# Optimization experiments

Hardware: AMD Instinct MI355X
Metric: run time of the kernel (lower is better)

The kernel has to match this reference:

```python
import jax, jax.numpy as jnp
import numpy as np
from jax import lax

EPS = 1e-4

def whatever_norm(z):
    m = jnp.mean(z, axis=-1, keepdims=True)
    v = jnp.var(z, axis=-1, keepdims=True)
    return (z - m) * lax.rsqrt(v + EPS)

def attend_layer(x_seq, speech, Ua_W, Ua_b, Wa_W, Wa_b, va_W, va_b, K, R, b):
    # x_seq: [B, T, U], speech: [B, Te, E]
    B = x_seq.shape[0]
    units = R.shape[0]
    enc = speech @ Ua_W + Ua_b  # [B, Te, U]  (Ua(speech_encode))

    def step(carry, x_t):
        h, c = carry
        s = h @ Wa_W + Wa_b                                   # Wa(states[0]) [B,U]
        logits = jnp.squeeze(jnp.tanh(s[:, None, :] + enc) @ va_W + va_b, -1)  # [B,Te]
        w = jax.nn.softmax(logits, axis=-1)
        ctx = jnp.einsum('bt,bte->be', w, speech)             # context [B,E]
        z = jnp.concatenate([x_t, ctx], axis=1) @ K + h @ R + b
        i, f, g, o = jnp.split(z, 4, axis=1)                  # keras gate order i,f,c,o
        i = jax.nn.sigmoid(i); f = jax.nn.sigmoid(f); o = jax.nn.sigmoid(o)
        c_new = f * c + i * jnp.tanh(g)
        h_new = o * jnp.tanh(c_new)
        return (h_new, c_new), h_new

    h0 = jnp.zeros((B, units), x_seq.dtype)
    _, ys = lax.scan(step, (h0, h0), jnp.swapaxes(x_seq, 0, 1))
    return jnp.swapaxes(ys, 0, 1)  # [B, T, U]


def setup_inputs() -> dict:
    key = jax.random.key(0)
    ks = iter(jax.random.split(key, 40))
    B, Td, Te, E, U, NC = 64, 512, 1024, 512, 256, 64
    g = lambda *s: (jax.random.normal(next(ks), s, dtype=jnp.float32) * (1.0 / np.sqrt(s[0])))
    inp = {
        'trans': jax.random.normal(next(ks), (B, Td, NC), dtype=jnp.float32),
        'speech': jax.random.normal(next(ks), (B, Te, E), dtype=jnp.float32),
        'emb_W': g(NC, U), 'emb_b': jnp.zeros((U,), jnp.float32),
    }
    for L in ('1', '2'):
        inp['Ua%s_W' % L] = g(E, U); inp['Ua%s_b' % L] = jnp.zeros((U,), jnp.float32)
        inp['Wa%s_W' % L] = g(U, U); inp['Wa%s_b' % L] = jnp.zeros((U,), jnp.float32)
        inp['va%s_W' % L] = g(U, 1); inp['va%s_b' % L] = jnp.zeros((1,), jnp.float32)
        inp['K%s' % L] = g(U + E, 4 * U)
        inp['R%s' % L] = g(U, 4 * U)
        # bias_initializer_two_cell: zeros for i, 2.0 for f, zeros for c and o
        inp['b%s' % L] = jnp.concatenate([
            jnp.zeros((U,)), 2.0 * jnp.ones((U,)), jnp.zeros((2 * U,))]).astype(jnp.float32)
    inp['m1_W'] = g(U, U); inp['m1_b'] = jnp.zeros((U,), jnp.float32)
    inp['m2_W'] = g(U, U); inp['m2_b'] = jnp.zeros((U,), jnp.float32)
    inp['d_W'] = g(U, NC); inp['d_b'] = jnp.zeros((NC,), jnp.float32)
    return inp


def reference(trans, speech, emb_W, emb_b,
              Ua1_W, Ua1_b, Wa1_W, Wa1_b, va1_W, va1_b, K1, R1, b1,
              Ua2_W, Ua2_b, Wa2_W, Wa2_b, va2_W, va2_b, K2, R2, b2,
              m1_W, m1_b, m2_W, m2_b, d_W, d_b):
    secrets = trans @ emb_W + emb_b
    out = attend_layer(secrets, speech, Ua1_W, Ua1_b, Wa1_W, Wa1_b, va1_W, va1_b, K1, R1, b1)
    out = whatever_norm(out)
    out = attend_layer(out, speech, Ua2_W, Ua2_b, Wa2_W, Wa2_b, va2_W, va2_b, K2, R2, b2)
    out = whatever_norm(out)
    out = whatever_norm(out @ m1_W + m1_b)
    out = whatever_norm(out @ m2_W + m2_b)
    return jax.nn.softmax(out @ d_W + d_b, axis=-1)
```

## Files before the change

kernel.cpp:

```cpp
#include <hip/hip_runtime.h>
#include <hip/hip_bf16.h>
#include <stdint.h>

#define B  64
#define TD 512
#define TE 1024
#define EE 512
#define UU 256

__device__ __forceinline__ float fexp2(float x){ return __builtin_amdgcn_exp2f(x); }
__device__ __forceinline__ float frcp_(float x){ return __builtin_amdgcn_rcpf(x); }
__device__ __forceinline__ float tanh_fast(float x){
  float e = fexp2(x * 2.885390082f);
  return 1.f - 2.f * frcp_(e + 1.f);
}
__device__ __forceinline__ float sigmoid_fast(float x){
  return frcp_(1.f + fexp2(-1.442695041f * x));
}
__device__ __forceinline__ unsigned short f2bf(float f){
  unsigned int u = __float_as_uint(f);
  u = (u + 0x7fffu + ((u >> 16) & 1u)) >> 16;
  return (unsigned short)u;
}
__device__ __forceinline__ float bflo(unsigned int w){ return __uint_as_float(w << 16); }
__device__ __forceinline__ float bfhi(unsigned int w){ return __uint_as_float(w & 0xffff0000u); }

__device__ __forceinline__ void gstore(float* p, float v){
  __hip_atomic_store(p, v, __ATOMIC_RELAXED, __HIP_MEMORY_SCOPE_SYSTEM);
}
__device__ __forceinline__ float gload(const float* p){
  return __hip_atomic_load(p, __ATOMIC_RELAXED, __HIP_MEMORY_SCOPE_SYSTEM);
}
__device__ __forceinline__ void drain_stores(){
  __atomic_signal_fence(__ATOMIC_SEQ_CST);
  __builtin_amdgcn_s_waitcnt(0);
  __atomic_signal_fence(__ATOMIC_SEQ_CST);
}

template<int NITER>
__device__ __forceinline__ void gate_accum8(const unsigned short* __restrict__ KRP,
    const float* catp, float* zb, int q8, int k0, int tid, int lane){
  const int c = tid & 15, kg = tid >> 4;
  const uint4* kp = (const uint4*)KRP + ((size_t)q8*1024 + k0 + kg*NITER)*16 + c;
  float a0=0.f,a1=0.f,a2=0.f,a3=0.f,a4=0.f,a5=0.f,a6=0.f,a7=0.f;
  #pragma unroll 4
  for (int i = 0; i < NITER; ++i){
    uint4 w = kp[(size_t)i*16];
    float ck = catp[k0 + kg*NITER + i];
    a0 += ck*bflo(w.x); a1 += ck*bfhi(w.x);
    a2 += ck*bflo(w.y); a3 += ck*bfhi(w.y);
    a4 += ck*bflo(w.z); a5 += ck*bfhi(w.z);
    a6 += ck*bflo(w.w); a7 += ck*bfhi(w.w);
  }
  a0 += __shfl_xor(a0, 16); a1 += __shfl_xor(a1, 16);
  a2 += __shfl_xor(a2, 16); a3 += __shfl_xor(a3, 16);
  a4 += __shfl_xor(a4, 16); a5 += __shfl_xor(a5, 16);
  a6 += __shfl_xor(a6, 16); a7 += __shfl_xor(a7, 16);
  a0 += __shfl_xor(a0, 32); a1 += __shfl_xor(a1, 32);
  a2 += __shfl_xor(a2, 32); a3 += __shfl_xor(a3, 32);
  a4 += __shfl_xor(a4, 32); a5 += __shfl_xor(a5, 32);
  a6 += __shfl_xor(a6, 32); a7 += __shfl_xor(a7, 32);
  if (lane < 16){
    atomicAdd(&zb[c*8+0], a0); atomicAdd(&zb[c*8+1], a1);
    atomicAdd(&zb[c*8+2], a2); atomicAdd(&zb[c*8+3], a3);
    atomicAdd(&zb[c*8+4], a4); atomicAdd(&zb[c*8+5], a5);
    atomicAdd(&zb[c*8+6], a6); atomicAdd(&zb[c*8+7], a7);
  }
}

__global__ void pack_bf16v(const float* __restrict__ in, unsigned short* __restrict__ out, int n4){
  int i = blockIdx.x * blockDim.x + threadIdx.x;
  int stride = gridDim.x * blockDim.x;
  for (; i < n4; i += stride){
    float4 v = ((const float4*)in)[i];
    ushort4 o;
    o.x = f2bf(v.x); o.y = f2bf(v.y); o.z = f2bf(v.z); o.w = f2bf(v.w);
    ((ushort4*)out)[i] = o;
  }
}

__global__ void pack_KRP(const float* __restrict__ K, const float* __restrict__ R,
                         unsigned short* __restrict__ KRP){
  int idx = blockIdx.x * 256 + threadIdx.x;
  int q8 = idx >> 17;
  int k  = (idx >> 7) & 1023;
  int jj = idx & 127;
  int J  = (jj >> 5)*256 + q8*32 + (jj & 31);
  float v = (k < 768) ? K[(size_t)k*1024 + J] : R[(size_t)(k - 768)*1024 + J];
  KRP[idx] = f2bf(v);
}

__global__ __launch_bounds__(256) void emb_gemm(const float* __restrict__ trans,
    const float* __restrict__ W, const float* __restrict__ bias, float* __restrict__ out){
  __shared__ __align__(16) float aT[64*20];
  const int row0 = blockIdx.x * 16;
  const int tid = threadIdx.x;
  {
    int r = tid >> 6, k = tid & 63;
    for (int rr = r; rr < 16; rr += 4)
      aT[k*20 + rr] = trans[(size_t)(row0 + rr)*64 + k];
  }
  __syncthreads();
  const int j = tid;
  float bj = bias[j];
  float acc[16];
  #pragma unroll
  for (int r = 0; r < 16; ++r) acc[r] = bj;
  for (int k = 0; k < 64; ++k){
    float w = W[(size_t)k*UU + j];
    const float4* a4 = (const float4*)(aT + k*20);
    float4 q0 = a4[0], q1 = a4[1], q2 = a4[2], q3 = a4[3];
    acc[0]+=q0.x*w;  acc[1]+=q0.y*w;  acc[2]+=q0.z*w;  acc[3]+=q0.w*w;
    acc[4]+=q1.x*w;  acc[5]+=q1.y*w;  acc[6]+=q1.z*w;  acc[7]+=q1.w*w;
    acc[8]+=q2.x*w;  acc[9]+=q2.y*w;  acc[10]+=q2.z*w; acc[11]+=q2.w*w;
    acc[12]+=q3.x*w; acc[13]+=q3.y*w; acc[14]+=q3.z*w; acc[15]+=q3.w*w;
  }
  #pragma unroll
  for (int r = 0; r < 16; ++r)
    out[(size_t)(row0 + r)*UU + j] = acc[r];
}

__global__ __launch_bounds__(256) void enc_gemm(const float* __restrict__ speech,
    const float* __restrict__ Ua, const float* __restrict__ Uab,
    unsigned short* __restrict__ enc){
  __shared__ __align__(16) float aT[512*20];
  const int wg = blockIdx.x;
  const int b = wg >> 6, tb = (wg & 63) * 16;
  const int tid = threadIdx.x;
  const float* sp = speech + ((size_t)b*TE + tb)*EE;
  for (int it = 0; it < 32; ++it){
    int idx = tid + 256*it;
    int te = idx >> 9, e = idx & 511;
    aT[e*20 + te] = sp[(size_t)te*EE + e];
  }
  __syncthreads();
  const int j = tid;
  float bj = Uab[j];
  float acc[16];
  #pragma unroll
  for (int r = 0; r < 16; ++r) acc[r] = bj;
  const float* up = Ua + j;
  for (int e = 0; e < 512; ++e){
    float w = up[(size_t)e*UU];
    const float4* a4 = (const float4*)(aT + e*20);
    float4 q0 = a4[0], q1 = a4[1], q2 = a4[2], q3 = a4[3];
    acc[0]+=q0.x*w;  acc[1]+=q0.y*w;  acc[2]+=q0.z*w;  acc[3]+=q0.w*w;
    acc[4]+=q1.x*w;  acc[5]+=q1.y*w;  acc[6]+=q1.z*w;  acc[7]+=q1.w*w;
    acc[8]+=q2.x*w;  acc[9]+=q2.y*w;  acc[10]+=q2.z*w; acc[11]+=q2.w*w;
    acc[12]+=q3.x*w; acc[13]+=q3.y*w; acc[14]+=q3.z*w; acc[15]+=q3.w*w;
  }
  unsigned short* op = enc + ((size_t)b*TE + tb)*UU + j;
  #pragma unroll
  for (int r = 0; r < 16; ++r) op[(size_t)r*UU] = f2bf(acc[r]);
}

__global__ __launch_bounds__(512)
__attribute__((amdgpu_waves_per_eu(4, 4)))
void scan_kernel(
    const float* __restrict__ x_seq, float* __restrict__ y_out,
    const unsigned short* __restrict__ enc, const unsigned short* __restrict__ speech,
    const unsigned short* __restrict__ KRP, const unsigned short* __restrict__ Wab,
    const float* __restrict__ Wa_b, const float* __restrict__ va,
    const float* __restrict__ gate_b,
    float* __restrict__ pctx_g, float* __restrict__ l_g, float* __restrict__ h_g,
    unsigned int* __restrict__ ctr){
  extern __shared__ __align__(16) unsigned short enc_l[];
  __shared__ float2 sva[256];
  __shared__ float cat[1024];
  __shared__ float c_lds[32];
  __shared__ float lds_logit4[512];
  __shared__ float p_lds[128];
  __shared__ float lds_pctx[512];
  __shared__ float zbuf[2][128];
  __shared__ float s_acc[256];
  __shared__ float red[16];
  __shared__ float nmi[2];

  const int tid = threadIdx.x;
  const int wg = blockIdx.x;
  const int b = wg >> 3, q8 = wg & 7;
  const int lane = tid & 63, wave = tid >> 6;
  unsigned int bar = 0;
  unsigned int* cptr = &ctr[b*16];

  {
    const uint4* ep4 = (const uint4*)(enc + ((size_t)b*TE + q8*128)*UU);
    #pragma unroll
    for (int i = 0; i < 8; ++i){
      int idx = tid + 512*i;
      int te_l = idx >> 5, ch = idx & 31;
      uint4 v = ep4[(size_t)te_l*32 + ch];
      *(uint4*)(enc_l + (size_t)te_l*264 + ch*8) = v;
    }
  }
  if (tid < 256){ sva[tid] = make_float2(Wa_b[tid], va[tid]); cat[768 + tid] = 0.f; }
  if (tid < 128){ zbuf[0][tid] = 0.f; zbuf[1][tid] = 0.f; }
  if (tid < 32) c_lds[tid] = 0.f;
  if (tid >= 256 && tid < 512)
    cat[tid - 256] = x_seq[((size_t)b*TD + 0)*UU + (tid - 256)];
  __syncthreads();
  gate_accum8<8>(KRP, cat, zbuf[0], q8, 0, tid, lane);

  for (int t = 0; t < TD; ++t){
    lds_pctx[tid] = 0.f;
    if (tid < 128) zbuf[(t+1)&1][tid] = 0.f;
    if (tid < 256) s_acc[tid] = 0.f;
    float xnext = 0.f;
    if (t < TD-1 && tid >= 256 && tid < 512)
      xnext = x_seq[((size_t)b*TD + t + 1)*UU + (tid - 256)];
    __syncthreads();

    {
      const int g = wave & 1, r = wave >> 1;
      const int te_l = g*64 + lane;
      const unsigned short* ep = enc_l + (size_t)te_l*264 + r*64;
      float acc = 0.f;
      #pragma unroll
      for (int c = 0; c < 8; ++c){
        uint4 v = *(const uint4*)(ep + c*8);
        const int ub = r*64 + c*8;
        unsigned int wv[4] = {v.x, v.y, v.z, v.w};
        #pragma unroll
        for (int i = 0; i < 4; ++i){
          float2 s0 = sva[ub + 2*i];
          float2 s1 = sva[ub + 2*i + 1];
          acc += s0.y * tanh_fast(s0.x + bflo(wv[i]));
          acc += s1.y * tanh_fast(s1.x + bfhi(wv[i]));
        }
      }
      lds_logit4[r*128 + te_l] = acc;
    }
    __syncthreads();

    if (tid < 128){
      float lg = lds_logit4[tid] + lds_logit4[128 + tid]
               + lds_logit4[256 + tid] + lds_logit4[384 + tid];
      float p = fexp2(lg * 1.442695041f);
      p_lds[tid] = p;
      float s = p;
      #pragma unroll
      for (int o = 32; o > 0; o >>= 1) s += __shfl_xor(s, o);
      if (lane == 0) red[wave] = s;
    }
    __syncthreads();

    {
      const int c = tid & 63, tg = tid >> 6;
      const uint4* sp4 = (const uint4*)speech + ((size_t)b*TE + q8*128 + tg*16)*64 + c;
      float a0=0.f,a1=0.f,a2=0.f,a3=0.f,a4=0.f,a5=0.f,a6=0.f,a7=0.f;
      #pragma unroll 4
      for (int i = 0; i < 16; ++i){
        uint4 w = sp4[(size_t)i*64];
        float p = p_lds[tg*16 + i];
        a0 += p*bflo(w.x); a1 += p*bfhi(w.x);
        a2 += p*bflo(w.y); a3 += p*bfhi(w.y);
        a4 += p*bflo(w.z); a5 += p*bfhi(w.z);
        a6 += p*bflo(w.w); a7 += p*bfhi(w.w);
      }
      atomicAdd(&lds_pctx[c*8+0], a0); atomicAdd(&lds_pctx[c*8+1], a1);
      atomicAdd(&lds_pctx[c*8+2], a2); atomicAdd(&lds_pctx[c*8+3], a3);
      atomicAdd(&lds_pctx[c*8+4], a4); atomicAdd(&lds_pctx[c*8+5], a5);
      atomicAdd(&lds_pctx[c*8+6], a6); atomicAdd(&lds_pctx[c*8+7], a7);
    }
    __syncthreads();
    gstore(&pctx_g[((size_t)(b*8 + q8))*512 + tid], lds_pctx[tid]);
    if (tid == 0)  gstore(&l_g[b*8 + q8], red[0] + red[1]);
    drain_stores();
    __syncthreads();
    bar += 8;
    if (tid == 0)
      __hip_atomic_fetch_add(cptr, 1u, __ATOMIC_RELAXED, __HIP_MEMORY_SCOPE_SYSTEM);

    gate_accum8<8>(KRP, cat, zbuf[t&1], q8, 768, tid, lane);

    if (t > 0){
      if (tid < 256){
        float hv = cat[768 + tid];
        float s1 = hv, s2 = hv*hv;
        #pragma unroll
        for (int o = 32; o > 0; o >>= 1){ s1 += __shfl_xor(s1, o); s2 += __shfl_xor(s2, o); }
        if (lane == 0){ red[wave*2] = s1; red[wave*2 + 1] = s2; }
      }
      __syncthreads();
      if (tid == 0){
        float m  = (red[0] + red[2] + red[4] + red[6]) * (1.f/256.f);
        float ms = (red[1] + red[3] + red[5] + red[7]) * (1.f/256.f);
        nmi[0] = m;
        nmi[1] = rsqrtf(ms - m*m + 1e-4f);
      }
      __syncthreads();
      if (tid < 32)
        y_out[((size_t)b*TD + (t-1))*UU + q8*32 + tid] =
            (cat[768 + q8*32 + tid] - nmi[0]) * nmi[1];
    }

    if (tid == 0){
      while (__hip_atomic_load(cptr, __ATOMIC_RELAXED, __HIP_MEMORY_SCOPE_SYSTEM) < bar)
        __builtin_amdgcn_s_sleep(2);
    }
    __syncthreads();

    {
      float lsum = 0.f;
      #pragma unroll
      for (int k = 0; k < 8; ++k) lsum += gload(&l_g[b*8 + k]);
      float linv = frcp_(lsum);
      float s0 = 0.f;
      #pragma unroll
      for (int k = 0; k < 8; ++k)
        s0 += gload(&pctx_g[((size_t)(b*8 + k))*512 + tid]);
      cat[256 + tid] = s0 * linv;
    }
    __syncthreads();

    gate_accum8<16>(KRP, cat, zbuf[t&1], q8, 256, tid, lane);
    __syncthreads();

    if (tid < 32){
      const int jj = q8*32 + tid;
      const float* zb = zbuf[t&1];
      float zi = zb[tid]      + gate_b[jj];
      float zf = zb[32 + tid] + gate_b[256 + jj];
      float zg = zb[64 + tid] + gate_b[512 + jj];
      float zo = zb[96 + tid] + gate_b[768 + jj];
      float cn = sigmoid_fast(zf) * c_lds[tid] + sigmoid_fast(zi) * tanh_fast(zg);
      c_lds[tid] = cn;
      gstore(&h_g[(size_t)b*UU + jj], sigmoid_fast(zo) * tanh_fast(cn));
    }
    if (t < TD-1 && tid >= 256 && tid < 512) cat[tid - 256] = xnext;
    drain_stores();
    __syncthreads();
    bar += 8;
    if (tid == 0)
      __hip_atomic_fetch_add(cptr, 1u, __ATOMIC_RELAXED, __HIP_MEMORY_SCOPE_SYSTEM);

    if (t < TD-1)
      gate_accum8<8>(KRP, cat, zbuf[(t+1)&1], q8, 0, tid, lane);

    if (tid == 0){
      while (__hip_atomic_load(cptr, __ATOMIC_RELAXED, __HIP_MEMORY_SCOPE_SYSTEM) < bar)
        __builtin_amdgcn_s_sleep(2);
    }
    __syncthreads();

    if (tid < 256) cat[768 + tid] = gload(&h_g[(size_t)b*UU + tid]);
    __syncthreads();

    if (t < TD - 1){
      {
        const int c = tid & 31, kg = tid >> 5;
        const uint4* wp = (const uint4*)Wab + (size_t)(kg*16)*32 + c;
        float a0=0.f,a1=0.f,a2=0.f,a3=0.f,a4=0.f,a5=0.f,a6=0.f,a7=0.f;
        #pragma unroll 4
        for (int i = 0; i < 16; ++i){
          uint4 w = wp[(size_t)i*32];
          float hk = cat[768 + kg*16 + i];
          a0 += hk*bflo(w.x); a1 += hk*bfhi(w.x);
          a2 += hk*bflo(w.y); a3 += hk*bfhi(w.y);
          a4 += hk*bflo(w.z); a5 += hk*bfhi(w.z);
          a6 += hk*bflo(w.w); a7 += hk*bfhi(w.w);
        }
        a0 += __shfl_xor(a0, 32); a1 += __shfl_xor(a1, 32);
        a2 += __shfl_xor(a2, 32); a3 += __shfl_xor(a3, 32);
        a4 += __shfl_xor(a4, 32); a5 += __shfl_xor(a5, 32);
        a6 += __shfl_xor(a6, 32); a7 += __shfl_xor(a7, 32);
        if (lane < 32){
          atomicAdd(&s_acc[c*8+0], a0); atomicAdd(&s_acc[c*8+1], a1);
          atomicAdd(&s_acc[c*8+2], a2); atomicAdd(&s_acc[c*8+3], a3);
          atomicAdd(&s_acc[c*8+4], a4); atomicAdd(&s_acc[c*8+5], a5);
          atomicAdd(&s_acc[c*8+6], a6); atomicAdd(&s_acc[c*8+7], a7);
        }
      }
      __syncthreads();
      if (tid < 256) sva[tid].x = Wa_b[tid] + s_acc[tid];
    }
    __syncthreads();
  }

  {
    if (tid < 256){
      float hv = cat[768 + tid];
      float s1 = hv, s2 = hv*hv;
      #pragma unroll
      for (int o = 32; o > 0; o >>= 1){ s1 += __shfl_xor(s1, o); s2 += __shfl_xor(s2, o); }
      if (lane == 0){ red[wave*2] = s1; red[wave*2 + 1] = s2; }
    }
    __syncthreads();
    if (tid == 0){
      float m  = (red[0] + red[2] + red[4] + red[6]) * (1.f/256.f);
      float ms = (red[1] + red[3] + red[5] + red[7]) * (1.f/256.f);
      nmi[0] = m;
      nmi[1] = rsqrtf(ms - m*m + 1e-4f);
    }
    __syncthreads();
    if (tid < 32)
      y_out[((size_t)b*TD + (TD-1))*UU + q8*32 + tid] =
          (cat[768 + q8*32 + tid] - nmi[0]) * nmi[1];
  }
}

__global__ __launch_bounds__(256) void head_kernel(const float* __restrict__ y2,
    const float* __restrict__ m1W, const float* __restrict__ m1b,
    const float* __restrict__ m2W, const float* __restrict__ m2b,
    const float* __restrict__ dW, const float* __restrict__ db,
    float* __restrict__ out){
  __shared__ __align__(16) float aT[256*20];
  __shared__ float t_lds[16*256];
  __shared__ float zl[16*64];
  __shared__ float mi[32];
  const int row0 = blockIdx.x * 16;
  const int tid = threadIdx.x;
  for (int it = 0; it < 16; ++it){
    int idx = tid + 256*it;
    int r = idx >> 8, k = idx & 255;
    aT[k*20 + r] = y2[(size_t)(row0 + r)*UU + k];
  }
  __syncthreads();

  #pragma unroll 1
  for (int pass = 0; pass < 2; ++pass){
    const float* Wp = pass ? m2W : m1W;
    const float* bp = pass ? m2b : m1b;
    const int j = tid;
    float bj = bp[j];
    float acc[16];
    #pragma unroll
    for (int r = 0; r < 16; ++r) acc[r] = bj;
    for (int k = 0; k < 256; ++k){
      float w = Wp[(size_t)k*UU + j];
      const float4* a4 = (const float4*)(aT + k*20);
      float4 q0 = a4[0], q1 = a4[1], q2 = a4[2], q3 = a4[3];
      acc[0]+=q0.x*w;  acc[1]+=q0.y*w;  acc[2]+=q0.z*w;  acc[3]+=q0.w*w;
      acc[4]+=q1.x*w;  acc[5]+=q1.y*w;  acc[6]+=q1.z*w;  acc[7]+=q1.w*w;
      acc[8]+=q2.x*w;  acc[9]+=q2.y*w;  acc[10]+=q2.z*w; acc[11]+=q2.w*w;
      acc[12]+=q3.x*w; acc[13]+=q3.y*w; acc[14]+=q3.z*w; acc[15]+=q3.w*w;
    }
    #pragma unroll
    for (int r = 0; r < 16; ++r) t_lds[r*256 + j] = acc[r];
    __syncthreads();
    {
      int r = tid >> 4, sg = tid & 15;
      float s1 = 0.f, s2 = 0.f;
      for (int c = 0; c < 16; ++c){
        float v = t_lds[r*256 + sg*16 + c];
        s1 += v; s2 += v*v;
      }
      for (int o = 1; o < 16; o <<= 1){ s1 += __shfl_xor(s1, o); s2 += __shfl_xor(s2, o); }
      if (sg == 0){
        float m = s1 * (1.f/256.f);
        float vv = s2 * (1.f/256.f) - m*m;
        mi[r*2] = m; mi[r*2+1] = rsqrtf(vv + 1e-4f);
      }
    }
    __syncthreads();
    {
      const int j2 = tid;
      #pragma unroll
      for (int r = 0; r < 16; ++r)
        aT[j2*20 + r] = (t_lds[r*256 + j2] - mi[r*2]) * mi[r*2+1];
    }
    __syncthreads();
  }

  for (int i = tid; i < 1024; i += 256) zl[i] = 0.f;
  __syncthreads();
  {
    const int j = tid & 63, kq = tid >> 6;
    float acc[16];
    #pragma unroll
    for (int r = 0; r < 16; ++r) acc[r] = 0.f;
    for (int k = 0; k < 64; ++k){
      float w = dW[(size_t)(kq*64 + k)*64 + j];
      const float4* a4 = (const float4*)(aT + (kq*64 + k)*20);
      float4 q0 = a4[0], q1 = a4[1], q2 = a4[2], q3 = a4[3];
      acc[0]+=q0.x*w;  acc[1]+=q0.y*w;  acc[2]+=q0.z*w;  acc[3]+=q0.w*w;
      acc[4]+=q1.x*w;  acc[5]+=q1.y*w;  acc[6]+=q1.z*w;  acc[7]+=q1.w*w;
      acc[8]+=q2.x*w;  acc[9]+=q2.y*w;  acc[10]+=q2.z*w; acc[11]+=q2.w*w;
      acc[12]+=q3.x*w; acc[13]+=q3.y*w; acc[14]+=q3.z*w; acc[15]+=q3.w*w;
    }
    #pragma unroll
    for (int r = 0; r < 16; ++r) atomicAdd(&zl[r*64 + j], acc[r]);
  }
  __syncthreads();
  if (tid < 16){
    const int r = tid;
    float mx = -1e30f;
    for (int j = 0; j < 64; ++j){ float v = zl[r*64 + j] + db[j]; zl[r*64 + j] = v; mx = fmaxf(mx, v); }
    float s = 0.f;
    for (int j = 0; j < 64; ++j){ float e = fexp2((zl[r*64 + j] - mx) * 1.442695041f); zl[r*64 + j] = e; s += e; }
    mi[r] = frcp_(s);
  }
  __syncthreads();
  for (int it = 0; it < 4; ++it){
    int idx = tid + 256*it;
    int r = idx >> 6, j = idx & 63;
    out[(size_t)(row0 + r)*64 + j] = zl[r*64 + j] * mi[r];
  }
}

#define OFF_SPEECH 0u
#define OFF_ENC    67108864u
#define OFF_KR     100663296u
#define OFF_WA     102760448u
#define OFF_X1     102891520u
#define OFF_Y1     136445952u
#define OFF_PCTX   170000384u
#define OFF_L      171048960u
#define OFF_H      171051008u
#define OFF_CTR    171116544u

#define DYN_LDS    67584

extern "C" void kernel_launch(void* const* d_in, const int* in_sizes, int n_in,
                              void* d_out, int out_size, void* d_ws, size_t ws_size,
                              hipStream_t stream){
  const float* trans  = (const float*)d_in[0];
  const float* speech = (const float*)d_in[1];
  const float* emb_W  = (const float*)d_in[2];
  const float* emb_b  = (const float*)d_in[3];
  const float* Ua_W[2]  = {(const float*)d_in[4],  (const float*)d_in[13]};
  const float* Ua_b[2]  = {(const float*)d_in[5],  (const float*)d_in[14]};
  const float* Wa_W[2]  = {(const float*)d_in[6],  (const float*)d_in[15]};
  const float* Wa_bv[2] = {(const float*)d_in[7],  (const float*)d_in[16]};
  const float* va_W[2]  = {(const float*)d_in[8],  (const float*)d_in[17]};
  const float* Kw[2]    = {(const float*)d_in[10], (const float*)d_in[19]};
  const float* Rw[2]    = {(const float*)d_in[11], (const float*)d_in[20]};
  const float* bw[2]    = {(const float*)d_in[12], (const float*)d_in[21]};
  const float* m1W = (const float*)d_in[22];
  const float* m1b = (const float*)d_in[23];
  const float* m2W = (const float*)d_in[24];
  const float* m2b = (const float*)d_in[25];
  const float* dW  = (const float*)d_in[26];
  const float* db  = (const float*)d_in[27];

  char* ws = (char*)d_ws;
  unsigned short* speech_bf = (unsigned short*)(ws + OFF_SPEECH);
  unsigned short* enc  = (unsigned short*)(ws + OFF_ENC);
  unsigned short* KRP  = (unsigned short*)(ws + OFF_KR);
  unsigned short* Wab  = (unsigned short*)(ws + OFF_WA);
  float* x1   = (float*)(ws + OFF_X1);
  float* y1   = (float*)(ws + OFF_Y1);
  float* pctx = (float*)(ws + OFF_PCTX);
  float* lg   = (float*)(ws + OFF_L);
  float* hg   = (float*)(ws + OFF_H);
  unsigned int* ctr = (unsigned int*)(ws + OFF_CTR);
  float* y2 = x1;

  hipFuncSetAttribute((const void*)scan_kernel,
                      hipFuncAttributeMaxDynamicSharedMemorySize, DYN_LDS);

  hipMemsetAsync(ctr, 0, 4096, stream);
  pack_bf16v<<<4096, 256, 0, stream>>>(speech, speech_bf, B*TE*EE/4);
  emb_gemm<<<2048, 256, 0, stream>>>(trans, emb_W, emb_b, x1);

  for (int L = 0; L < 2; ++L){
    enc_gemm<<<4096, 256, 0, stream>>>(speech, Ua_W[L], Ua_b[L], enc);
    pack_KRP<<<4096, 256, 0, stream>>>(Kw[L], Rw[L], KRP);
    pack_bf16v<<<64, 256, 0, stream>>>(Wa_W[L], Wab, UU*UU/4);
    if (L == 1) hipMemsetAsync(ctr, 0, 4096, stream);
    scan_kernel<<<512, 512, DYN_LDS, stream>>>(L == 0 ? x1 : y1, L == 0 ? y1 : y2,
        enc, speech_bf, KRP, Wab, Wa_bv[L], va_W[L], bw[L], pctx, lg, hg, ctr);
  }

  head_kernel<<<2048, 256, 0, stream>>>(y2, m1W, m1b, m2W, m2b, dW, db, (float*)d_out);
  (void)in_sizes; (void)n_in; (void)out_size; (void)ws_size;
}
```

Before: 39.77 ms.

## Replace counter barrier with per-block flags, atomic context reduction, and K-weight prefetch

Replaces the shared atomic-increment barrier counter with per-workgroup flag words that each block stores and eight lanes poll. Partial context and softmax denominators are now accumulated with global atomics into double-buffered accumulators, so each block reads one reduced value instead of summing eight partials. The double buffer is zeroed by one block each step. The K weights for the context-gate matmul are prefetched into registers before the barrier wait, hiding load latency behind the spin. Costs are global atomic contention, higher register pressure from the 16-entry uint4 prefetch, and ordering subtleties in the buffer zeroing.

```diff
diff --git a/kernel.cpp b/kernel.cpp
--- a/kernel.cpp
+++ b/kernel.cpp
@@ -29,6 +29,12 @@
   __hip_atomic_store(p, v, __ATOMIC_RELAXED, __HIP_MEMORY_SCOPE_SYSTEM);
 }
 __device__ __forceinline__ float gload(const float* p){
+  return __hip_atomic_load(p, __ATOMIC_RELAXED, __HIP_MEMORY_SCOPE_SYSTEM);
+}
+__device__ __forceinline__ void gstore_u(unsigned int* p, unsigned int v){
+  __hip_atomic_store(p, v, __ATOMIC_RELAXED, __HIP_MEMORY_SCOPE_SYSTEM);
+}
+__device__ __forceinline__ unsigned int gload_u(const unsigned int* p){
   return __hip_atomic_load(p, __ATOMIC_RELAXED, __HIP_MEMORY_SCOPE_SYSTEM);
 }
 __device__ __forceinline__ void drain_stores(){
@@ -162,8 +168,8 @@
     const unsigned short* __restrict__ KRP, const unsigned short* __restrict__ Wab,
     const float* __restrict__ Wa_b, const float* __restrict__ va,
     const float* __restrict__ gate_b,
-    float* __restrict__ pctx_g, float* __restrict__ l_g, float* __restrict__ h_g,
-    unsigned int* __restrict__ ctr){
+    float* __restrict__ ctx_acc, float* __restrict__ l_acc, float* __restrict__ h_g,
+    unsigned int* __restrict__ flg){
   extern __shared__ __align__(16) unsigned short enc_l[];
   __shared__ float2 sva[256];
   __shared__ float cat[1024];
@@ -181,7 +187,7 @@
   const int b = wg >> 3, q8 = wg & 7;
   const int lane = tid & 63, wave = tid >> 6;
   unsigned int bar = 0;
-  unsigned int* cptr = &ctr[b*16];
+  unsigned int* fbase = &flg[b*8];
 
   {
     const uint4* ep4 = (const uint4*)(enc + ((size_t)b*TE + q8*128)*UU);
@@ -263,15 +269,27 @@
       atomicAdd(&lds_pctx[c*8+6], a6); atomicAdd(&lds_pctx[c*8+7], a7);
     }
     __syncthreads();
-    gstore(&pctx_g[((size_t)(b*8 + q8))*512 + tid], lds_pctx[tid]);
-    if (tid == 0)  gstore(&l_g[b*8 + q8], red[0] + red[1]);
+    atomicAdd(&ctx_acc[((size_t)b*2 + (t&1))*512 + tid], lds_pctx[tid]);
+    if (tid == 0) atomicAdd(&l_acc[b*2 + (t&1)], red[0] + red[1]);
     drain_stores();
     __syncthreads();
-    bar += 8;
-    if (tid == 0)
-      __hip_atomic_fetch_add(cptr, 1u, __ATOMIC_RELAXED, __HIP_MEMORY_SCOPE_SYSTEM);
+    bar += 1;
+    if (tid == 0) gstore_u(&fbase[q8], bar);
 
     gate_accum8<8>(KRP, cat, zbuf[t&1], q8, 768, tid, lane);
+
+    if (q8 == 0){
+      gstore(&ctx_acc[((size_t)b*2 + ((t+1)&1))*512 + tid], 0.f);
+      if (tid == 0) gstore(&l_acc[b*2 + ((t+1)&1)], 0.f);
+    }
+
+    uint4 pf[16];
+    {
+      const int c = tid & 15, kg = tid >> 4;
+      const uint4* kp = (const uint4*)KRP + ((size_t)q8*1024 + 256 + kg*16)*16 + c;
+      #pragma unroll
+      for (int i = 0; i < 16; ++i) pf[i] = kp[(size_t)i*16];
+    }
 
     if (t > 0){
       if (tid < 256){
@@ -294,26 +312,45 @@
             (cat[768 + q8*32 + tid] - nmi[0]) * nmi[1];
     }
 
-    if (tid == 0){
-      while (__hip_atomic_load(cptr, __ATOMIC_RELAXED, __HIP_MEMORY_SCOPE_SYSTEM) < bar)
-        __builtin_amdgcn_s_sleep(2);
+    if (tid < 8){
+      while (gload_u(&fbase[tid]) < bar) __builtin_amdgcn_s_sleep(2);
     }
     __syncthreads();
 
     {
-      float lsum = 0.f;
+      float linv = frcp_(gload(&l_acc[b*2 + (t&1)]));
+      cat[256 + tid] = gload(&ctx_acc[((size_t)b*2 + (t&1))*512 + tid]) * linv;
+    }
+    __syncthreads();
+
+    {
+      const int c = tid & 15, kg = tid >> 4;
+      float a0=0.f,a1=0.f,a2=0.f,a3=0.f,a4=0.f,a5=0.f,a6=0.f,a7=0.f;
       #pragma unroll
-      for (int k = 0; k < 8; ++k) lsum += gload(&l_g[b*8 + k]);
-      float linv = frcp_(lsum);
-      float s0 = 0.f;
-      #pragma unroll
-      for (int k = 0; k < 8; ++k)
-        s0 += gload(&pctx_g[((size_t)(b*8 + k))*512 + tid]);
-      cat[256 + tid] = s0 * linv;
-    }
-    __syncthreads();
-
-    gate_accum8<16>(KRP, cat, zbuf[t&1], q8, 256, tid, lane);
+      for (int i = 0; i < 16; ++i){
+        uint4 w = pf[i];
+        float ck = cat[256 + kg*16 + i];
+        a0 += ck*bflo(w.x); a1 += ck*bfhi(w.x);
+        a2 += ck*bflo(w.y); a3 += ck*bfhi(w.y);
+        a4 += ck*bflo(w.z); a5 += ck*bfhi(w.z);
+        a6 += ck*bflo(w.w); a7 += ck*bfhi(w.w);
+      }
+      a0 += __shfl_xor(a0, 16); a1 += __shfl_xor(a1, 16);
+      a2 += __shfl_xor(a2, 16); a3 += __shfl_xor(a3, 16);
+      a4 += __shfl_xor(a4, 16); a5 += __shfl_xor(a5, 16);
+      a6 += __shfl_xor(a6, 16); a7 += __shfl_xor(a7, 16);
+      a0 += __shfl_xor(a0, 32); a1 += __shfl_xor(a1, 32);
+      a2 += __shfl_xor(a2, 32); a3 += __shfl_xor(a3, 32);
+      a4 += __shfl_xor(a4, 32); a5 += __shfl_xor(a5, 32);
+      a6 += __shfl_xor(a6, 32); a7 += __shfl_xor(a7, 32);
+      float* zb = zbuf[t&1];
+      if (lane < 16){
+        atomicAdd(&zb[c*8+0], a0); atomicAdd(&zb[c*8+1], a1);
+        atomicAdd(&zb[c*8+2], a2); atomicAdd(&zb[c*8+3], a3);
+        atomicAdd(&zb[c*8+4], a4); atomicAdd(&zb[c*8+5], a5);
+        atomicAdd(&zb[c*8+6], a6); atomicAdd(&zb[c*8+7], a7);
+      }
+    }
     __syncthreads();
 
     if (tid < 32){
@@ -330,16 +367,14 @@
     if (t < TD-1 && tid >= 256 && tid < 512) cat[tid - 256] = xnext;
     drain_stores();
     __syncthreads();
-    bar += 8;
-    if (tid == 0)
-      __hip_atomic_fetch_add(cptr, 1u, __ATOMIC_RELAXED, __HIP_MEMORY_SCOPE_SYSTEM);
+    bar += 1;
+    if (tid == 0) gstore_u(&fbase[q8], bar);
 
     if (t < TD-1)
       gate_accum8<8>(KRP, cat, zbuf[(t+1)&1], q8, 0, tid, lane);
 
-    if (tid == 0){
-      while (__hip_atomic_load(cptr, __ATOMIC_RELAXED, __HIP_MEMORY_SCOPE_SYSTEM) < bar)
-        __builtin_amdgcn_s_sleep(2);
+    if (tid < 8){
+      while (gload_u(&fbase[tid]) < bar) __builtin_amdgcn_s_sleep(2);
     }
     __syncthreads();
 
@@ -505,7 +540,7 @@
 #define OFF_X1     102891520u
 #define OFF_Y1     136445952u
 #define OFF_PCTX   170000384u
-#define OFF_L      171048960u
+#define OFF_LACC   170262528u
 #define OFF_H      171051008u
 #define OFF_CTR    171116544u
 
@@ -540,16 +575,15 @@
   unsigned short* Wab  = (unsigned short*)(ws + OFF_WA);
   float* x1   = (float*)(ws + OFF_X1);
   float* y1   = (float*)(ws + OFF_Y1);
-  float* pctx = (float*)(ws + OFF_PCTX);
-  float* lg   = (float*)(ws + OFF_L);
+  float* ctxa = (float*)(ws + OFF_PCTX);
+  float* lacc = (float*)(ws + OFF_LACC);
   float* hg   = (float*)(ws + OFF_H);
-  unsigned int* ctr = (unsigned int*)(ws + OFF_CTR);
+  unsigned int* flg = (unsigned int*)(ws + OFF_CTR);
   float* y2 = x1;
 
   hipFuncSetAttribute((const void*)scan_kernel,
                       hipFuncAttributeMaxDynamicSharedMemorySize, DYN_LDS);
 
-  hipMemsetAsync(ctr, 0, 4096, stream);
   pack_bf16v<<<4096, 256, 0, stream>>>(speech, speech_bf, B*TE*EE/4);
   emb_gemm<<<2048, 256, 0, stream>>>(trans, emb_W, emb_b, x1);
 
@@ -557,9 +591,10 @@
     enc_gemm<<<4096, 256, 0, stream>>>(speech, Ua_W[L], Ua_b[L], enc);
     pack_KRP<<<4096, 256, 0, stream>>>(Kw[L], Rw[L], KRP);
     pack_bf16v<<<64, 256, 0, stream>>>(Wa_W[L], Wab, UU*UU/4);
-    if (L == 1) hipMemsetAsync(ctr, 0, 4096, stream);
+    hipMemsetAsync(flg, 0, 4096, stream);
+    hipMemsetAsync(ctxa, 0, 262656, stream);
     scan_kernel<<<512, 512, DYN_LDS, stream>>>(L == 0 ? x1 : y1, L == 0 ? y1 : y2,
-        enc, speech_bf, KRP, Wab, Wa_bv[L], va_W[L], bw[L], pctx, lg, hg, ctr);
+        enc, speech_bf, KRP, Wab, Wa_bv[L], va_W[L], bw[L], ctxa, lacc, hg, flg);
   }
 
   head_kernel<<<2048, 256, 0, stream>>>(y2, m1W, m1b, m2W, m2b, dW, db, (float*)d_out);
```

Result: slower. 63.93 ms (+60.8%).
